# Performance work log

Measured on AMD Instinct MI355X. Metric: run time of the kernel, lower is better.

Reference implementation:

```python
import math
import jax, jax.numpy as jnp
import numpy as np

DIM = 512; DEPTH = 12; HEADS = 8; DIM_HEAD = 64
INNER = HEADS * DIM_HEAD
FF_INNER = 4 * DIM
B = 8192
NUM_TIMESTEPS = 1000
SCALE = 16.0  # cosine_sim_scale
ROT_DIM = 32  # RotaryEmbedding(dim=min(32, dim_head))
NUM_BUCKETS = 32; MAX_DISTANCE = 128


def layer_norm(x, g, eps=1e-5):
    mean = jnp.mean(x, axis=-1, keepdims=True)
    var = jnp.mean((x - mean) ** 2, axis=-1, keepdims=True)  # unbiased=False
    return (x - mean) * jax.lax.rsqrt(var + eps) * g


def l2norm(t):
    n = jnp.linalg.norm(t, axis=-1, keepdims=True)
    return t / jnp.maximum(n, 1e-12)


def rotary_freqs(n):
    inv = 1.0 / (10000.0 ** (jnp.arange(0, ROT_DIM, 2, dtype=jnp.float32) / ROT_DIM))
    f = jnp.arange(n, dtype=jnp.float32)[:, None] * inv[None, :]  # (n, ROT_DIM//2)
    return jnp.repeat(f, 2, axis=-1)  # (n, ROT_DIM), interleaved pairs


def rotate_half(x):
    x1 = x[..., 0::2]; x2 = x[..., 1::2]
    return jnp.stack((-x2, x1), axis=-1).reshape(x.shape)


def apply_rotary(t, freqs):
    tr, tp = t[..., :ROT_DIM], t[..., ROT_DIM:]
    tr = tr * jnp.cos(freqs) + rotate_half(tr) * jnp.sin(freqs)
    return jnp.concatenate([tr, tp], axis=-1)


def rel_pos_bias(i, j, emb):
    rel = jnp.arange(j)[None, :] - jnp.arange(i)[:, None]
    n = jnp.maximum(-rel, 0)
    max_exact = NUM_BUCKETS // 2
    nf = jnp.maximum(n, 1).astype(jnp.float32)
    val_large = max_exact + (jnp.log(nf / max_exact) / math.log(MAX_DISTANCE / max_exact) * (NUM_BUCKETS - max_exact)).astype(jnp.int32)
    val_large = jnp.minimum(val_large, NUM_BUCKETS - 1)
    bucket = jnp.where(n < max_exact, n, val_large)
    return emb[bucket].transpose(2, 0, 1)  # (h, i, j)


def setup_inputs() -> dict:
    key = jax.random.key(0)
    ks = jax.random.split(key, 13)
    w = 0.02
    return {
        "image_embed": jax.random.normal(ks[0], (B, DIM), jnp.float32),
        "text_embed": jax.random.normal(ks[1], (B, DIM), jnp.float32),
        "timesteps": jax.random.randint(ks[2], (B,), 0, NUM_TIMESTEPS),
        "time_emb_table": jax.random.normal(ks[3], (NUM_TIMESTEPS, DIM)) * w,
        "learned_query": jax.random.normal(ks[4], (DIM,)),
        "rel_emb": jax.random.normal(ks[5], (NUM_BUCKETS, HEADS)) * w,
        "attn_norm_g": jnp.ones((DEPTH, DIM)),
        "Wq": jax.random.normal(ks[6], (DEPTH, DIM, INNER)) * w,
        "Wkv": jax.random.normal(ks[7], (DEPTH, DIM, 2 * DIM_HEAD)) * w,
        "null_kv": jax.random.normal(ks[8], (DEPTH, 2, DIM_HEAD)),
        "Wo": jax.random.normal(ks[9], (DEPTH, INNER, DIM)) * w,
        "attn_out_norm_g": jnp.ones((DEPTH, DIM)),
        "ff_norm_g": jnp.ones((DEPTH, DIM)),
        "Wff1": jax.random.normal(ks[10], (DEPTH, DIM, 2 * FF_INNER)) * w,
        "Wff2": jax.random.normal(ks[11], (DEPTH, FF_INNER, DIM)) * w,
        "final_norm_g": jnp.ones((DIM,)),
        "Wproj": jax.random.normal(ks[12], (DIM, DIM)) * w,
    }


def reference(image_embed, text_embed, timesteps, time_emb_table, learned_query, rel_emb,
              attn_norm_g, Wq, Wkv, null_kv, Wo, attn_out_norm_g,
              ff_norm_g, Wff1, Wff2, final_norm_g, Wproj):
    b = image_embed.shape[0]
    # token sequence: [text_embed, time_embed, image_embed, learned_query] -> (b, 4, dim)
    tokens = jnp.concatenate([
        text_embed[:, None, :],
        time_emb_table[timesteps][:, None, :],
        image_embed[:, None, :],
        jnp.broadcast_to(learned_query, (b, 1, DIM)),
    ], axis=1)
    n = tokens.shape[1]
    bias = rel_pos_bias(n, n + 1, rel_emb)            # (h, n, n+1)
    freqs = rotary_freqs(n)                           # (n, ROT_DIM)
    causal = jnp.triu(jnp.ones((n, n + 1), dtype=bool), k=2)
    neg = -jnp.finfo(jnp.float32).max
    sqrt_scale = math.sqrt(SCALE)

    x = tokens
    for l in range(DEPTH):
        # --- Attention ---
        h = layer_norm(x, attn_norm_g[l])
        q = (h @ Wq[l]).reshape(b, n, HEADS, DIM_HEAD).transpose(0, 2, 1, 3) * SCALE
        kv = h @ Wkv[l]
        k, v = kv[..., :DIM_HEAD], kv[..., DIM_HEAD:]  # single-head kv (b, n, d)
        q = apply_rotary(q, freqs)
        k = apply_rotary(k, freqs)
        nk = jnp.broadcast_to(null_kv[l, 0], (b, 1, DIM_HEAD))
        nv = jnp.broadcast_to(null_kv[l, 1], (b, 1, DIM_HEAD))
        k = jnp.concatenate([nk, k], axis=1)
        v = jnp.concatenate([nv, v], axis=1)
        q = l2norm(q) * sqrt_scale
        k = l2norm(k) * sqrt_scale
        sim = jnp.einsum('bhid,bjd->bhij', q, k) + bias[None]
        sim = jnp.where(causal[None, None], neg, sim)
        attn = jax.nn.softmax(sim.astype(jnp.float32), axis=-1).astype(sim.dtype)
        out = jnp.einsum('bhij,bjd->bhid', attn, v).transpose(0, 2, 1, 3).reshape(b, n, INNER)
        x = x + layer_norm(out @ Wo[l], attn_out_norm_g[l])
        # --- SwiGLU FFN ---
        h = layer_norm(x, ff_norm_g[l])
        hg = h @ Wff1[l]
        a, g = hg[..., :FF_INNER], hg[..., FF_INNER:]
        x = x + (a * jax.nn.silu(g)) @ Wff2[l]

    x = layer_norm(x, final_norm_g) @ Wproj
    return x[:, -1, :]  # predicted image embed from learned query position
```

## Files before the change

kernel.cpp:

```cpp
#include <hip/hip_runtime.h>

typedef __bf16 bf16x8 __attribute__((ext_vector_type(8)));
typedef __bf16 bf16x2 __attribute__((ext_vector_type(2)));
typedef float  f32x4  __attribute__((ext_vector_type(4)));
typedef unsigned short u16;

#define BATCH   8192
#define NTOK    4
#define ROWS    (BATCH*NTOK)
#define DIM     512
#define HEADS   8
#define DH      64
#define FFI     2048
#define DEPTH   12
#define LN_EPS  1e-5f

static const size_t OFF_WQKV = 0;
static const size_t SZ_WQKV  = 12ull*640*512*2;
static const size_t OFF_WTO  = OFF_WQKV + SZ_WQKV;
static const size_t SZ_WTO   = 12ull*512*512*2;
static const size_t OFF_WTF1 = OFF_WTO + SZ_WTO;
static const size_t SZ_WTF1  = 12ull*4096*512*2;
static const size_t OFF_WTF2 = OFF_WTF1 + SZ_WTF1;
static const size_t SZ_WTF2  = 12ull*512*2048*2;
static const size_t OFF_WTP  = OFF_WTF2 + SZ_WTF2;
static const size_t SZ_WTP   = 512ull*512*2;
static const size_t OFF_X    = OFF_WTP + SZ_WTP;
static const size_t OFF_H    = OFF_X    + (size_t)ROWS*DIM*4;
static const size_t OFF_QKV  = OFF_H    + (size_t)ROWS*DIM*2;
static const size_t OFF_AO   = OFF_QKV  + (size_t)ROWS*640*2;
static const size_t OFF_FLAG = OFF_AO   + (size_t)ROWS*DIM*2;
static const size_t WS_NEED  = OFF_FLAG + 256;

__device__ __forceinline__ float ldf(const void* p, size_t i, bool b16) {
  return b16 ? (float)((const __bf16*)p)[i] : ((const float*)p)[i];
}

__device__ __forceinline__ void gld_lds16(const void* g, void* l) {
  __builtin_amdgcn_global_load_lds((const __attribute__((address_space(1))) void*)g,
                                   (__attribute__((address_space(3))) void*)l, 16, 0, 0);
}

__device__ __forceinline__ float wave_sum(float v) {
  #pragma unroll
  for (int o = 32; o > 0; o >>= 1) v += __shfl_xor(v, o, 64);
  return v;
}

__device__ __forceinline__ void block_reduce2(float& a, float& b, float* sm) {
  #pragma unroll
  for (int o = 32; o > 0; o >>= 1) { a += __shfl_down(a, o, 64); b += __shfl_down(b, o, 64); }
  int lane = threadIdx.x & 63, w = threadIdx.x >> 6;
  __syncthreads();
  if (lane == 0) { sm[w] = a; sm[4+w] = b; }
  __syncthreads();
  a = sm[0]+sm[1]+sm[2]+sm[3];
  b = sm[4]+sm[5]+sm[6]+sm[7];
}

__global__ void detect_dtype(const unsigned int* __restrict__ w, int* __restrict__ flag) {
  __shared__ int cnt[4];
  int t = threadIdx.x;
  int c = 0;
  for (int i = t; i < 2048; i += 256) {
    unsigned int v = w[i];
    unsigned int lo = v & 0xFFFFu, hi = v >> 16;
    int elo = (int)((lo >> 7) & 0xFF), ehi = (int)((hi >> 7) & 0xFF);
    bool okl = (lo == 0u) || (elo >= 100 && elo <= 140);
    bool okh = (hi == 0u) || (ehi >= 100 && ehi <= 140);
    if (okl && okh) c++;
  }
  #pragma unroll
  for (int o = 32; o > 0; o >>= 1) c += __shfl_down(c, o, 64);
  if ((t & 63) == 0) cnt[t >> 6] = c;
  __syncthreads();
  if (t == 0) flag[0] = (cnt[0] + cnt[1] + cnt[2] + cnt[3] > 1024) ? 1 : 0;
}

__global__ void transpose_any(const void* __restrict__ in, u16* __restrict__ out,
                              int K, int N, size_t out_zsz, int rowoff, int mode,
                              const int* __restrict__ flag) {
  bool b16 = flag[0] != 0;
  __shared__ u16 tile[32][33];
  size_t iboff = (size_t)blockIdx.z * K * N;
  size_t oboff = (size_t)blockIdx.z * out_zsz;
  int n0 = blockIdx.x * 32, k0 = blockIdx.y * 32;
  int tx = threadIdx.x, ty = threadIdx.y;
  #pragma unroll
  for (int r = 0; r < 4; r++) {
    float v = ldf(in, iboff + (size_t)(k0 + ty*4 + r) * N + n0 + tx, b16);
    __bf16 bv = (__bf16)v;
    tile[ty*4+r][tx] = __builtin_bit_cast(u16, bv);
  }
  __syncthreads();
  int rbase;
  if (mode == 0) rbase = rowoff + n0;
  else {
    int s = (n0 >= 2048) ? 1 : 0;
    int np = n0 - s*2048;
    rbase = (np >> 7)*256 + ((np >> 5) & 3)*64 + s*32;
  }
  #pragma unroll
  for (int r = 0; r < 4; r++)
    out[oboff + (size_t)(rbase + ty*4 + r) * K + k0 + tx] = tile[tx][ty*4+r];
}

__global__ void build_tokens(const void* __restrict__ text, const void* __restrict__ img,
                             const int* __restrict__ ts, const void* __restrict__ table,
                             const void* __restrict__ lq, float* __restrict__ x,
                             const int* __restrict__ flag) {
  bool b16 = flag[0] != 0;
  int b = blockIdx.x, t = threadIdx.x;
  float* xr = x + (size_t)b * NTOK * DIM;
  int tsb = ts[b];
  for (int e = t; e < DIM; e += 256) {
    xr[e]         = ldf(text,  (size_t)b * DIM + e, b16);
    xr[DIM + e]   = ldf(table, (size_t)tsb * DIM + e, b16);
    xr[2*DIM + e] = ldf(img,   (size_t)b * DIM + e, b16);
    xr[3*DIM + e] = ldf(lq,    (size_t)e, b16);
  }
}

__global__ void ln_f32_bf16(const float* __restrict__ x, const void* __restrict__ g, size_t goff,
                            __bf16* __restrict__ out, const int* __restrict__ flag) {
  bool b16 = flag[0] != 0;
  __shared__ float sm[8];
  int row = blockIdx.x, t = threadIdx.x;
  float2 v = ((const float2*)(x + (size_t)row * DIM))[t];
  float s = v.x + v.y, s2 = v.x*v.x + v.y*v.y;
  block_reduce2(s, s2, sm);
  float mean = s * (1.f/DIM);
  float var  = s2 * (1.f/DIM) - mean*mean;
  float rs = rsqrtf(var + LN_EPS);
  float g0 = ldf(g, goff + 2*t, b16), g1 = ldf(g, goff + 2*t + 1, b16);
  bf16x2 o2 = { (__bf16)((v.x-mean)*rs*g0), (__bf16)((v.y-mean)*rs*g1) };
  ((bf16x2*)(out + (size_t)row * DIM))[t] = o2;
}

__global__ void ln_add_ln(const __bf16* __restrict__ y,
                          const void* __restrict__ g1, size_t g1off,
                          const void* __restrict__ g2, size_t g2off,
                          float* __restrict__ x, __bf16* __restrict__ h,
                          const int* __restrict__ flag) {
  bool b16 = flag[0] != 0;
  __shared__ float sm[8];
  int row = blockIdx.x, t = threadIdx.x;
  bf16x2 yv = ((const bf16x2*)(y + (size_t)row * DIM))[t];
  float v0 = (float)yv[0], v1 = (float)yv[1];
  float s = v0 + v1, s2 = v0*v0 + v1*v1;
  block_reduce2(s, s2, sm);
  float mean = s * (1.f/DIM);
  float var  = s2 * (1.f/DIM) - mean*mean;
  float rs = rsqrtf(var + LN_EPS);
  float ga = ldf(g1, g1off + 2*t, b16), gb = ldf(g1, g1off + 2*t + 1, b16);
  float2* xr = (float2*)(x + (size_t)row * DIM);
  float2 xv = xr[t];
  xv.x += (v0-mean)*rs*ga;
  xv.y += (v1-mean)*rs*gb;
  xr[t] = xv;
  float s_  = xv.x + xv.y, s2_ = xv.x*xv.x + xv.y*xv.y;
  block_reduce2(s_, s2_, sm);
  float mean2 = s_ * (1.f/DIM);
  float var2  = s2_ * (1.f/DIM) - mean2*mean2;
  float rs2 = rsqrtf(var2 + LN_EPS);
  float gc = ldf(g2, g2off + 2*t, b16), gd = ldf(g2, g2off + 2*t + 1, b16);
  bf16x2 o2 = { (__bf16)((xv.x-mean2)*rs2*gc), (__bf16)((xv.y-mean2)*rs2*gd) };
  ((bf16x2*)(h + (size_t)row * DIM))[t] = o2;
}

__global__ void ln_final(const float* __restrict__ x, const void* __restrict__ g,
                         __bf16* __restrict__ out, const int* __restrict__ flag) {
  bool b16 = flag[0] != 0;
  __shared__ float sm[8];
  int b = blockIdx.x, t = threadIdx.x;
  int row = b*NTOK + 3;
  float2 v = ((const float2*)(x + (size_t)row * DIM))[t];
  float s = v.x + v.y, s2 = v.x*v.x + v.y*v.y;
  block_reduce2(s, s2, sm);
  float mean = s * (1.f/DIM);
  float var  = s2 * (1.f/DIM) - mean*mean;
  float rs = rsqrtf(var + LN_EPS);
  float g0 = ldf(g, (size_t)2*t, b16), g1 = ldf(g, (size_t)2*t + 1, b16);
  bf16x2 o2 = { (__bf16)((v.x-mean)*rs*g0), (__bf16)((v.y-mean)*rs*g1) };
  ((bf16x2*)(out + (size_t)b * DIM))[t] = o2;
}

template<int MODE>
__global__ __launch_bounds__(256) void gemm_bt(
    const __bf16* __restrict__ A, int lda,
    const __bf16* __restrict__ B, int ldb,
    void* __restrict__ Cv, int ldc, int K, const int* __restrict__ flag)
{
  __shared__ __bf16 As[128*64];
  __shared__ __bf16 Bs[128*64];
  const int tid = threadIdx.x;
  const int bx = blockIdx.x, by = blockIdx.y;
  const int wave = tid >> 6, lane = tid & 63;
  const int wr = wave >> 1, wc = wave & 1;
  const __bf16* Ab = A + (size_t)by * 128 * lda;
  const __bf16* Bb = B + (size_t)bx * 128 * ldb;
  f32x4 acc[4][4] = {};
  const int srow = tid >> 3;
  const int scs  = ((tid & 7) ^ (srow & 7)) * 8;
  const int lr = lane & 15, lc = lane >> 4;
  for (int k0 = 0; k0 < K; k0 += 64) {
    __syncthreads();
    #pragma unroll
    for (int s = 0; s < 4; s++) {
      gld_lds16(Ab + (size_t)(s*32 + srow)*lda + k0 + scs, (char*)As + s*4096 + wave*1024);
      gld_lds16(Bb + (size_t)(s*32 + srow)*ldb + k0 + scs, (char*)Bs + s*4096 + wave*1024);
    }
    __syncthreads();
    #pragma unroll
    for (int kk = 0; kk < 2; kk++) {
      bf16x8 af[4], bq[4];
      #pragma unroll
      for (int m = 0; m < 4; m++)
        af[m] = *(const bf16x8*)(As + (wr*64 + m*16 + lr)*64 + (((kk*4 + lc) ^ (lr & 7)) * 8));
      #pragma unroll
      for (int n = 0; n < 4; n++)
        bq[n] = *(const bf16x8*)(Bs + (wc*64 + n*16 + lr)*64 + (((kk*4 + lc) ^ (lr & 7)) * 8));
      #pragma unroll
      for (int m = 0; m < 4; m++)
        #pragma unroll
        for (int n = 0; n < 4; n++)
          acc[m][n] = __builtin_amdgcn_mfma_f32_16x16x32_bf16(af[m], bq[n], acc[m][n], 0, 0, 0);
    }
  }
  const int row0 = by*128 + wr*64 + (lane >> 4)*4;
  const int col0 = bx*128 + wc*64 + (lane & 15);
  if (MODE == 0) {
    __bf16* Cb = (__bf16*)Cv;
    #pragma unroll
    for (int m = 0; m < 4; m++)
      #pragma unroll
      for (int rr = 0; rr < 4; rr++) {
        size_t ro = (size_t)(row0 + m*16 + rr) * ldc + col0;
        #pragma unroll
        for (int n = 0; n < 4; n++) Cb[ro + n*16] = (__bf16)acc[m][n][rr];
      }
  } else {
    bool b16o = flag[0] != 0;
    __bf16* Cb = (__bf16*)Cv;
    float*  Cf = (float*)Cv;
    #pragma unroll
    for (int m = 0; m < 4; m++)
      #pragma unroll
      for (int rr = 0; rr < 4; rr++) {
        size_t ro = (size_t)(row0 + m*16 + rr) * ldc + col0;
        #pragma unroll
        for (int n = 0; n < 4; n++) {
          float val = acc[m][n][rr];
          if (b16o) Cb[ro + n*16] = (__bf16)val; else Cf[ro + n*16] = val;
        }
      }
  }
}

template<int BROWS, int EPI>
__global__ __launch_bounds__(512, 2) void gemm8(
    const __bf16* __restrict__ A, int lda,
    const __bf16* __restrict__ B, int ldb,
    void* __restrict__ Cv, int ldc, int K)
{
  constexpr int UNITS = (BROWS == 256) ? 4 : 3;
  constexpr int WCN   = (BROWS == 256) ? 4 : 2;
  constexpr int M_FR  = (BROWS == 256) ? 8 : 4;
  constexpr int QM    = M_FR / 4;
  __shared__ char ldsmem[2][(256 + BROWS) * 128];

  const int tid = threadIdx.x;
  const int wid = tid >> 6, lane = tid & 63;
  const int wr = wid / WCN, wc = wid % WCN;
  const int lr = lane & 15, lc = lane >> 4;
  const int sr = tid >> 3;
  const int cs = ((tid & 7) ^ (sr & 7)) * 8;
  const int bx = blockIdx.x, by = blockIdx.y;

  const __bf16* Ab = A + (size_t)by * 256 * lda;
  const __bf16* Bb = B + (size_t)bx * BROWS * ldb;

  f32x4 acc[M_FR][4] = {};
  const int NT = K >> 6;

  char* lds0 = ldsmem[0];
  char* lds1 = ldsmem[1];

  auto stage_unit = [&](int p, int kt, int u) {
    char* base = (p ? lds1 : lds0);
    if (u < 2) {
      const __bf16* s = Ab + (size_t)(u*128 + sr) * lda + kt*64 + cs;
      char* d = base + u*16384 + (wid << 10);
      gld_lds16(s, d);
      gld_lds16(s + (size_t)64 * lda, d + 8192);
    } else {
      const __bf16* s = Bb + (size_t)((u-2)*128 + sr) * ldb + kt*64 + cs;
      char* d = base + 32768 + (u-2)*16384 + (wid << 10);
      gld_lds16(s, d);
      gld_lds16(s + (size_t)64 * ldb, d + 8192);
    }
  };

  #pragma unroll
  for (int u = 0; u < UNITS; u++) stage_unit(0, 0, u);

  const int NIT = NT >> 1;
  for (int i = 0; i < NIT; i++) {
    const int t1 = 2*i + 1;
    const int t2 = (2*i + 2 < NT) ? (2*i + 2) : 0;
    #pragma unroll
    for (int hfl = 0; hfl < 2; hfl++) {
      char* cbase = hfl ? lds1 : lds0;
      const int sp = hfl ^ 1;
      const int st = hfl ? t2 : t1;
      bf16x8 bfr[4][2];
      #pragma unroll
      for (int q = 0; q < 4; q++) {
        if (q < UNITS) stage_unit(sp, st, q);
        if (q == 0) {
          asm volatile("s_waitcnt vmcnt(2)" ::: "memory");
          asm volatile("s_barrier" ::: "memory");
          #pragma unroll
          for (int f = 0; f < 4; f++)
            #pragma unroll
            for (int kk = 0; kk < 2; kk++) {
              int row = wc*64 + f*16 + lr;
              int ch = (kk*4 + lc) ^ (lr & 7);
              bfr[f][kk] = *(const bf16x8*)(cbase + 32768 + row*128 + ch*16);
            }
        }
        bf16x8 afr[QM][2];
        #pragma unroll
        for (int m2 = 0; m2 < QM; m2++)
          #pragma unroll
          for (int kk = 0; kk < 2; kk++) {
            int row = wr*(M_FR*16) + (q*QM + m2)*16 + lr;
            int ch = (kk*4 + lc) ^ (lr & 7);
            afr[m2][kk] = *(const bf16x8*)(cbase + row*128 + ch*16);
          }
        __builtin_amdgcn_s_setprio(1);
        #pragma unroll
        for (int m2 = 0; m2 < QM; m2++)
          #pragma unroll
          for (int n = 0; n < 4; n++)
            #pragma unroll
            for (int kk = 0; kk < 2; kk++)
              acc[q*QM + m2][n] = __builtin_amdgcn_mfma_f32_16x16x32_bf16(
                  afr[m2][kk], bfr[n][kk], acc[q*QM + m2][n], 0, 0, 0);
        __builtin_amdgcn_s_setprio(0);
        asm volatile("s_barrier" ::: "memory");
      }
    }
  }

  if (EPI == 1) {
    __bf16* Ob = (__bf16*)Cv;
    const int colb = bx*128 + wc*32 + lr;
    const int rowb = by*256 + wr*128 + lc*4;
    #pragma unroll
    for (int m = 0; m < M_FR; m++)
      #pragma unroll
      for (int rr = 0; rr < 4; rr++) {
        size_t ro = (size_t)(rowb + m*16 + rr) * ldc;
        #pragma unroll
        for (int fa = 0; fa < 2; fa++) {
          float a = acc[m][fa][rr], g = acc[m][fa+2][rr];
          Ob[ro + colb + fa*16] = (__bf16)(a * g / (1.f + __expf(-g)));
        }
      }
  } else {
    float* Xf = (float*)Cv;
    const int colb = bx*BROWS + wc*64 + lr;
    const int rowb = by*256 + wr*(M_FR*16) + lc*4;
    #pragma unroll
    for (int m = 0; m < M_FR; m++)
      #pragma unroll
      for (int rr = 0; rr < 4; rr++) {
        size_t ro = (size_t)(rowb + m*16 + rr) * ldc;
        #pragma unroll
        for (int n = 0; n < 4; n++) Xf[ro + colb + n*16] += acc[m][n][rr];
      }
  }
}

__global__ __launch_bounds__(256) void attn_kernel(
    const __bf16* __restrict__ qkv,
    const void* __restrict__ nkv_all, int layer, const void* __restrict__ rel_emb,
    __bf16* __restrict__ ao, const int* __restrict__ flag)
{
  bool b16 = flag[0] != 0;
  int gw = blockIdx.x * 4 + (threadIdx.x >> 6);
  int lane = threadIdx.x & 63;
  int b = gw >> 3, h = gw & 7;
  int d = lane;
  bool rot = d < 32;
  int j2 = d >> 1;
  float inv = __expf(-(float)(2*j2) * (1.f/32.f) * 9.210340371976184f);

  float sn[4], cn[4];
  #pragma unroll
  for (int t2 = 0; t2 < 4; t2++) __sincosf((float)t2 * inv, &sn[t2], &cn[t2]);
  float rb[4];
  #pragma unroll
  for (int t2 = 0; t2 < 4; t2++) rb[t2] = ldf(rel_emb, (size_t)t2 * 8 + h, b16);

  float q[4];
  #pragma unroll
  for (int i = 0; i < 4; i++) {
    float v = (float)qkv[((size_t)(b*NTOK + i)) * 640 + h*DH + d];
    float p = __shfl_xor(v, 1, 64);
    if (rot) v = (d & 1) ? (v*cn[i] + p*sn[i]) : (v*cn[i] - p*sn[i]);
    q[i] = v;
  }
  #pragma unroll
  for (int i = 0; i < 4; i++) {
    float nrm = sqrtf(wave_sum(q[i]*q[i]));
    q[i] = q[i] / fmaxf(nrm, 1e-12f);
  }

  float kk[5], vv[5];
  kk[0] = ldf(nkv_all, (size_t)layer*128 + d, b16);
  vv[0] = ldf(nkv_all, (size_t)layer*128 + 64 + d, b16);
  #pragma unroll
  for (int j = 1; j < 5; j++) {
    const __bf16* base = qkv + ((size_t)(b*NTOK + j - 1)) * 640 + 512;
    float v = (float)base[d];
    vv[j] = (float)base[64 + d];
    float p = __shfl_xor(v, 1, 64);
    if (rot) v = (d & 1) ? (v*cn[j-1] + p*sn[j-1]) : (v*cn[j-1] - p*sn[j-1]);
    kk[j] = v;
  }
  #pragma unroll
  for (int j = 0; j < 5; j++) {
    float nrm = sqrtf(wave_sum(kk[j]*kk[j]));
    kk[j] = kk[j] / fmaxf(nrm, 1e-12f);
  }

  #pragma unroll
  for (int i = 0; i < 4; i++) {
    float sim[5];
    #pragma unroll
    for (int j = 0; j < 5; j++) {
      if (j > i + 1) break;
      float p = wave_sum(q[i] * kk[j]);
      sim[j] = p * 16.f + rb[(i - j > 0) ? (i - j) : 0];
    }
    float m = sim[0];
    #pragma unroll
    for (int j = 1; j < 5; j++) { if (j > i + 1) break; m = fmaxf(m, sim[j]); }
    float Z = 0.f, o = 0.f;
    #pragma unroll
    for (int j = 0; j < 5; j++) {
      if (j > i + 1) break;
      float e = __expf(sim[j] - m);
      Z += e; o += e * vv[j];
    }
    ao[((size_t)(b*NTOK + i)) * DIM + h*DH + d] = (__bf16)(o / Z);
  }
}

extern "C" void kernel_launch(void* const* d_in, const int* in_sizes, int n_in,
                              void* d_out, int out_size, void* d_ws, size_t ws_size,
                              hipStream_t stream) {
  const void* image_embed     = d_in[0];
  const void* text_embed      = d_in[1];
  const int*  timesteps       = (const int*)d_in[2];
  const void* time_table      = d_in[3];
  const void* learned_query   = d_in[4];
  const void* rel_emb         = d_in[5];
  const void* attn_norm_g     = d_in[6];
  const void* Wq              = d_in[7];
  const void* Wkv             = d_in[8];
  const void* null_kv         = d_in[9];
  const void* Wo              = d_in[10];
  const void* attn_out_norm_g = d_in[11];
  const void* ff_norm_g       = d_in[12];
  const void* Wff1            = d_in[13];
  const void* Wff2            = d_in[14];
  const void* final_norm_g    = d_in[15];
  const void* Wproj           = d_in[16];

  if (ws_size < WS_NEED) return;

  char* ws = (char*)d_ws;
  __bf16* wqkv = (__bf16*)(ws + OFF_WQKV);
  __bf16* wto  = (__bf16*)(ws + OFF_WTO);
  __bf16* wtf1 = (__bf16*)(ws + OFF_WTF1);
  __bf16* wtf2 = (__bf16*)(ws + OFF_WTF2);
  __bf16* wtp  = (__bf16*)(ws + OFF_WTP);
  float*  x    = (float*) (ws + OFF_X);
  __bf16* h    = (__bf16*)(ws + OFF_H);
  __bf16* qkv  = (__bf16*)(ws + OFF_QKV);
  __bf16* ao   = (__bf16*)(ws + OFF_AO);
  __bf16* act  = (__bf16*)(ws + OFF_QKV);
  int*    flag = (int*)   (ws + OFF_FLAG);

  detect_dtype<<<1, 256, 0, stream>>>((const unsigned int*)Wq, flag);

  dim3 tb(32, 8);
  transpose_any<<<dim3(16, 16, 12),  tb, 0, stream>>>(Wq,   (u16*)wqkv, 512,  512,  640ull*512, 0,   0, flag);
  transpose_any<<<dim3(4,  16, 12),  tb, 0, stream>>>(Wkv,  (u16*)wqkv, 512,  128,  640ull*512, 512, 0, flag);
  transpose_any<<<dim3(16, 16, 12),  tb, 0, stream>>>(Wo,   (u16*)wto,  512,  512,  512ull*512, 0,   0, flag);
  transpose_any<<<dim3(128,16, 12),  tb, 0, stream>>>(Wff1, (u16*)wtf1, 512,  4096, 4096ull*512,0,   1, flag);
  transpose_any<<<dim3(16, 64, 12),  tb, 0, stream>>>(Wff2, (u16*)wtf2, 2048, 512,  512ull*2048,0,   0, flag);
  transpose_any<<<dim3(16, 16, 1),   tb, 0, stream>>>(Wproj,(u16*)wtp,  512,  512,  512ull*512, 0,   0, flag);

  build_tokens<<<BATCH, 256, 0, stream>>>(text_embed, image_embed, timesteps, time_table,
                                          learned_query, x, flag);

  for (int l = 0; l < DEPTH; l++) {
    const __bf16* wqkv_l = wqkv + (size_t)l * 640 * 512;
    const __bf16* wto_l  = wto  + (size_t)l * 512 * 512;
    const __bf16* wtf1_l = wtf1 + (size_t)l * 4096 * 512;
    const __bf16* wtf2_l = wtf2 + (size_t)l * 512 * 2048;

    ln_f32_bf16<<<ROWS, 256, 0, stream>>>(x, attn_norm_g, (size_t)l*DIM, h, flag);
    gemm_bt<0><<<dim3(5, ROWS/128), 256, 0, stream>>>(h, DIM, wqkv_l, 512, qkv, 640, 512, flag);
    attn_kernel<<<BATCH*HEADS/4, 256, 0, stream>>>(qkv, null_kv, l, rel_emb, ao, flag);
    gemm_bt<0><<<dim3(4, ROWS/128), 256, 0, stream>>>(ao, DIM, wto_l, 512, qkv , DIM, 512, flag);
    ln_add_ln<<<ROWS, 256, 0, stream>>>(qkv , attn_out_norm_g, (size_t)l*DIM,
                                        ff_norm_g, (size_t)l*DIM, x, h, flag);

    for (int c = 0; c < 2; c++) {
      const __bf16* hc = h + (size_t)c * 16384 * DIM;
      float*        xc = x + (size_t)c * 16384 * DIM;
      gemm8<256,1><<<dim3(16, 64), 512, 0, stream>>>(hc, DIM, wtf1_l, 512, act, FFI, 512);
      gemm8<128,2><<<dim3(4, 64), 512, 0, stream>>>(act, FFI, wtf2_l, FFI, xc, DIM, 2048);
    }
  }

  ln_final<<<BATCH, 256, 0, stream>>>(x, final_norm_g, ao , flag);
  gemm_bt<2><<<dim3(4, BATCH/128), 256, 0, stream>>>(ao, DIM, wtp, 512, d_out, DIM, 512, flag);
}
```

Baseline: 6.172 ms.

## Replace small gemm_bt with gemm8 tiles and vectorize attention to 16 lanes per head

Removes the 128x128 gemm_bt kernel and routes the QKV, output-projection and final projection GEMMs through the larger 256x128 gemm8 kernel, adding bf16 and flag-dependent output epilogues. The attention kernel now handles each (batch, head) with a 16-lane group, each lane holding 4 elements, so reductions take 4 shuffle steps instead of 6 and loads and stores are 8-byte vectors. The aim is better GEMM efficiency from larger tiles with pipelined loads, and less shuffle and launch overhead in attention. Larger tiles mean fewer blocks for these small-N GEMMs, which may hurt occupancy.

```diff
diff --git a/kernel.cpp b/kernel.cpp
--- a/kernel.cpp
+++ b/kernel.cpp
@@ -1,6 +1,7 @@
 #include <hip/hip_runtime.h>
 
 typedef __bf16 bf16x8 __attribute__((ext_vector_type(8)));
+typedef __bf16 bf16x4 __attribute__((ext_vector_type(4)));
 typedef __bf16 bf16x2 __attribute__((ext_vector_type(2)));
 typedef float  f32x4  __attribute__((ext_vector_type(4)));
 typedef unsigned short u16;
@@ -41,9 +42,9 @@
                                    (__attribute__((address_space(3))) void*)l, 16, 0, 0);
 }
 
-__device__ __forceinline__ float wave_sum(float v) {
-  #pragma unroll
-  for (int o = 32; o > 0; o >>= 1) v += __shfl_xor(v, o, 64);
+__device__ __forceinline__ float gsum16(float v) {
+  #pragma unroll
+  for (int o = 8; o > 0; o >>= 1) v += __shfl_xor(v, o, 64);
   return v;
 }
 
@@ -185,83 +186,11 @@
   ((bf16x2*)(out + (size_t)b * DIM))[t] = o2;
 }
 
-template<int MODE>
-__global__ __launch_bounds__(256) void gemm_bt(
-    const __bf16* __restrict__ A, int lda,
-    const __bf16* __restrict__ B, int ldb,
-    void* __restrict__ Cv, int ldc, int K, const int* __restrict__ flag)
-{
-  __shared__ __bf16 As[128*64];
-  __shared__ __bf16 Bs[128*64];
-  const int tid = threadIdx.x;
-  const int bx = blockIdx.x, by = blockIdx.y;
-  const int wave = tid >> 6, lane = tid & 63;
-  const int wr = wave >> 1, wc = wave & 1;
-  const __bf16* Ab = A + (size_t)by * 128 * lda;
-  const __bf16* Bb = B + (size_t)bx * 128 * ldb;
-  f32x4 acc[4][4] = {};
-  const int srow = tid >> 3;
-  const int scs  = ((tid & 7) ^ (srow & 7)) * 8;
-  const int lr = lane & 15, lc = lane >> 4;
-  for (int k0 = 0; k0 < K; k0 += 64) {
-    __syncthreads();
-    #pragma unroll
-    for (int s = 0; s < 4; s++) {
-      gld_lds16(Ab + (size_t)(s*32 + srow)*lda + k0 + scs, (char*)As + s*4096 + wave*1024);
-      gld_lds16(Bb + (size_t)(s*32 + srow)*ldb + k0 + scs, (char*)Bs + s*4096 + wave*1024);
-    }
-    __syncthreads();
-    #pragma unroll
-    for (int kk = 0; kk < 2; kk++) {
-      bf16x8 af[4], bq[4];
-      #pragma unroll
-      for (int m = 0; m < 4; m++)
-        af[m] = *(const bf16x8*)(As + (wr*64 + m*16 + lr)*64 + (((kk*4 + lc) ^ (lr & 7)) * 8));
-      #pragma unroll
-      for (int n = 0; n < 4; n++)
-        bq[n] = *(const bf16x8*)(Bs + (wc*64 + n*16 + lr)*64 + (((kk*4 + lc) ^ (lr & 7)) * 8));
-      #pragma unroll
-      for (int m = 0; m < 4; m++)
-        #pragma unroll
-        for (int n = 0; n < 4; n++)
-          acc[m][n] = __builtin_amdgcn_mfma_f32_16x16x32_bf16(af[m], bq[n], acc[m][n], 0, 0, 0);
-    }
-  }
-  const int row0 = by*128 + wr*64 + (lane >> 4)*4;
-  const int col0 = bx*128 + wc*64 + (lane & 15);
-  if (MODE == 0) {
-    __bf16* Cb = (__bf16*)Cv;
-    #pragma unroll
-    for (int m = 0; m < 4; m++)
-      #pragma unroll
-      for (int rr = 0; rr < 4; rr++) {
-        size_t ro = (size_t)(row0 + m*16 + rr) * ldc + col0;
-        #pragma unroll
-        for (int n = 0; n < 4; n++) Cb[ro + n*16] = (__bf16)acc[m][n][rr];
-      }
-  } else {
-    bool b16o = flag[0] != 0;
-    __bf16* Cb = (__bf16*)Cv;
-    float*  Cf = (float*)Cv;
-    #pragma unroll
-    for (int m = 0; m < 4; m++)
-      #pragma unroll
-      for (int rr = 0; rr < 4; rr++) {
-        size_t ro = (size_t)(row0 + m*16 + rr) * ldc + col0;
-        #pragma unroll
-        for (int n = 0; n < 4; n++) {
-          float val = acc[m][n][rr];
-          if (b16o) Cb[ro + n*16] = (__bf16)val; else Cf[ro + n*16] = val;
-        }
-      }
-  }
-}
-
 template<int BROWS, int EPI>
 __global__ __launch_bounds__(512, 2) void gemm8(
     const __bf16* __restrict__ A, int lda,
     const __bf16* __restrict__ B, int ldb,
-    void* __restrict__ Cv, int ldc, int K)
+    void* __restrict__ Cv, int ldc, int K, const int* __restrict__ flag)
 {
   constexpr int UNITS = (BROWS == 256) ? 4 : 3;
   constexpr int WCN   = (BROWS == 256) ? 4 : 2;
@@ -368,7 +297,7 @@
           Ob[ro + colb + fa*16] = (__bf16)(a * g / (1.f + __expf(-g)));
         }
       }
-  } else {
+  } else if (EPI == 2) {
     float* Xf = (float*)Cv;
     const int colb = bx*BROWS + wc*64 + lr;
     const int rowb = by*256 + wr*(M_FR*16) + lc*4;
@@ -380,6 +309,35 @@
         #pragma unroll
         for (int n = 0; n < 4; n++) Xf[ro + colb + n*16] += acc[m][n][rr];
       }
+  } else if (EPI == 0) {
+    __bf16* Cb = (__bf16*)Cv;
+    const int colb = bx*BROWS + wc*64 + lr;
+    const int rowb = by*256 + wr*(M_FR*16) + lc*4;
+    #pragma unroll
+    for (int m = 0; m < M_FR; m++)
+      #pragma unroll
+      for (int rr = 0; rr < 4; rr++) {
+        size_t ro = (size_t)(rowb + m*16 + rr) * ldc;
+        #pragma unroll
+        for (int n = 0; n < 4; n++) Cb[ro + colb + n*16] = (__bf16)acc[m][n][rr];
+      }
+  } else {
+    bool b16o = flag[0] != 0;
+    __bf16* Cb = (__bf16*)Cv;
+    float*  Cf = (float*)Cv;
+    const int colb = bx*BROWS + wc*64 + lr;
+    const int rowb = by*256 + wr*(M_FR*16) + lc*4;
+    #pragma unroll
+    for (int m = 0; m < M_FR; m++)
+      #pragma unroll
+      for (int rr = 0; rr < 4; rr++) {
+        size_t ro = (size_t)(rowb + m*16 + rr) * ldc;
+        #pragma unroll
+        for (int n = 0; n < 4; n++) {
+          float val = acc[m][n][rr];
+          if (b16o) Cb[ro + colb + n*16] = (__bf16)val; else Cf[ro + colb + n*16] = val;
+        }
+      }
   }
 }
 
@@ -389,51 +347,74 @@
     __bf16* __restrict__ ao, const int* __restrict__ flag)
 {
   bool b16 = flag[0] != 0;
-  int gw = blockIdx.x * 4 + (threadIdx.x >> 6);
-  int lane = threadIdx.x & 63;
-  int b = gw >> 3, h = gw & 7;
-  int d = lane;
-  bool rot = d < 32;
-  int j2 = d >> 1;
-  float inv = __expf(-(float)(2*j2) * (1.f/32.f) * 9.210340371976184f);
-
-  float sn[4], cn[4];
-  #pragma unroll
-  for (int t2 = 0; t2 < 4; t2++) __sincosf((float)t2 * inv, &sn[t2], &cn[t2]);
+  const int tid = threadIdx.x;
+  const int w = tid >> 6, l = tid & 63;
+  const int g = l >> 4, c = l & 15;
+  const int bh = blockIdx.x * 16 + w * 4 + g;
+  const int b = bh >> 3, h = bh & 7;
+  const bool rot = (c < 8);
+
+  const float LN1E4_32 = 9.210340371976184f * (1.f/32.f);
+  float inv0 = __expf(-(float)(4*c)     * LN1E4_32);
+  float inv1 = __expf(-(float)(4*c + 2) * LN1E4_32);
+  float cs0[4], sn0[4], cs1[4], sn1[4];
+  #pragma unroll
+  for (int t = 0; t < 4; t++) {
+    __sincosf((float)t * inv0, &sn0[t], &cs0[t]);
+    __sincosf((float)t * inv1, &sn1[t], &cs1[t]);
+  }
   float rb[4];
   #pragma unroll
-  for (int t2 = 0; t2 < 4; t2++) rb[t2] = ldf(rel_emb, (size_t)t2 * 8 + h, b16);
-
-  float q[4];
+  for (int t = 0; t < 4; t++) rb[t] = ldf(rel_emb, (size_t)t * 8 + h, b16);
+
+  float q[4][4];
   #pragma unroll
   for (int i = 0; i < 4; i++) {
-    float v = (float)qkv[((size_t)(b*NTOK + i)) * 640 + h*DH + d];
-    float p = __shfl_xor(v, 1, 64);
-    if (rot) v = (d & 1) ? (v*cn[i] + p*sn[i]) : (v*cn[i] - p*sn[i]);
-    q[i] = v;
+    bf16x4 qv = *(const bf16x4*)(qkv + ((size_t)(b*NTOK + i)) * 640 + h*DH + c*4);
+    float v0 = (float)qv[0], v1 = (float)qv[1], v2 = (float)qv[2], v3 = (float)qv[3];
+    if (rot) {
+      float n0 = v0*cs0[i] - v1*sn0[i], n1 = v1*cs0[i] + v0*sn0[i];
+      float n2 = v2*cs1[i] - v3*sn1[i], n3 = v3*cs1[i] + v2*sn1[i];
+      v0 = n0; v1 = n1; v2 = n2; v3 = n3;
+    }
+    q[i][0] = v0; q[i][1] = v1; q[i][2] = v2; q[i][3] = v3;
   }
   #pragma unroll
   for (int i = 0; i < 4; i++) {
-    float nrm = sqrtf(wave_sum(q[i]*q[i]));
-    q[i] = q[i] / fmaxf(nrm, 1e-12f);
-  }
-
-  float kk[5], vv[5];
-  kk[0] = ldf(nkv_all, (size_t)layer*128 + d, b16);
-  vv[0] = ldf(nkv_all, (size_t)layer*128 + 64 + d, b16);
+    float ss = q[i][0]*q[i][0] + q[i][1]*q[i][1] + q[i][2]*q[i][2] + q[i][3]*q[i][3];
+    float r = 1.f / fmaxf(sqrtf(gsum16(ss)), 1e-12f);
+    #pragma unroll
+    for (int e = 0; e < 4; e++) q[i][e] *= r;
+  }
+
+  float kk[5][4], vv[5][4];
+  #pragma unroll
+  for (int e = 0; e < 4; e++) {
+    kk[0][e] = ldf(nkv_all, (size_t)layer*128 + c*4 + e, b16);
+    vv[0][e] = ldf(nkv_all, (size_t)layer*128 + 64 + c*4 + e, b16);
+  }
   #pragma unroll
   for (int j = 1; j < 5; j++) {
     const __bf16* base = qkv + ((size_t)(b*NTOK + j - 1)) * 640 + 512;
-    float v = (float)base[d];
-    vv[j] = (float)base[64 + d];
-    float p = __shfl_xor(v, 1, 64);
-    if (rot) v = (d & 1) ? (v*cn[j-1] + p*sn[j-1]) : (v*cn[j-1] - p*sn[j-1]);
-    kk[j] = v;
+    bf16x4 kv4 = *(const bf16x4*)(base + c*4);
+    bf16x4 vv4 = *(const bf16x4*)(base + 64 + c*4);
+    float v0 = (float)kv4[0], v1 = (float)kv4[1], v2 = (float)kv4[2], v3 = (float)kv4[3];
+    if (rot) {
+      int t = j - 1;
+      float n0 = v0*cs0[t] - v1*sn0[t], n1 = v1*cs0[t] + v0*sn0[t];
+      float n2 = v2*cs1[t] - v3*sn1[t], n3 = v3*cs1[t] + v2*sn1[t];
+      v0 = n0; v1 = n1; v2 = n2; v3 = n3;
+    }
+    kk[j][0] = v0; kk[j][1] = v1; kk[j][2] = v2; kk[j][3] = v3;
+    #pragma unroll
+    for (int e = 0; e < 4; e++) vv[j][e] = (float)vv4[e];
   }
   #pragma unroll
   for (int j = 0; j < 5; j++) {
-    float nrm = sqrtf(wave_sum(kk[j]*kk[j]));
-    kk[j] = kk[j] / fmaxf(nrm, 1e-12f);
+    float ss = kk[j][0]*kk[j][0] + kk[j][1]*kk[j][1] + kk[j][2]*kk[j][2] + kk[j][3]*kk[j][3];
+    float r = 1.f / fmaxf(sqrtf(gsum16(ss)), 1e-12f);
+    #pragma unroll
+    for (int e = 0; e < 4; e++) kk[j][e] *= r;
   }
 
   #pragma unroll
@@ -442,20 +423,23 @@
     #pragma unroll
     for (int j = 0; j < 5; j++) {
       if (j > i + 1) break;
-      float p = wave_sum(q[i] * kk[j]);
-      sim[j] = p * 16.f + rb[(i - j > 0) ? (i - j) : 0];
+      float pp = q[i][0]*kk[j][0] + q[i][1]*kk[j][1] + q[i][2]*kk[j][2] + q[i][3]*kk[j][3];
+      sim[j] = 16.f * gsum16(pp) + rb[(i - j > 0) ? (i - j) : 0];
     }
     float m = sim[0];
     #pragma unroll
     for (int j = 1; j < 5; j++) { if (j > i + 1) break; m = fmaxf(m, sim[j]); }
-    float Z = 0.f, o = 0.f;
+    float Z = 0.f, o0 = 0.f, o1 = 0.f, o2 = 0.f, o3 = 0.f;
     #pragma unroll
     for (int j = 0; j < 5; j++) {
       if (j > i + 1) break;
       float e = __expf(sim[j] - m);
-      Z += e; o += e * vv[j];
-    }
-    ao[((size_t)(b*NTOK + i)) * DIM + h*DH + d] = (__bf16)(o / Z);
+      Z += e;
+      o0 += e * vv[j][0]; o1 += e * vv[j][1]; o2 += e * vv[j][2]; o3 += e * vv[j][3];
+    }
+    float rz = 1.f / Z;
+    bf16x4 ov = { (__bf16)(o0*rz), (__bf16)(o1*rz), (__bf16)(o2*rz), (__bf16)(o3*rz) };
+    *(bf16x4*)(ao + ((size_t)(b*NTOK + i)) * DIM + h*DH + c*4) = ov;
   }
 }
 
@@ -515,20 +499,20 @@
     const __bf16* wtf2_l = wtf2 + (size_t)l * 512 * 2048;
 
     ln_f32_bf16<<<ROWS, 256, 0, stream>>>(x, attn_norm_g, (size_t)l*DIM, h, flag);
-    gemm_bt<0><<<dim3(5, ROWS/128), 256, 0, stream>>>(h, DIM, wqkv_l, 512, qkv, 640, 512, flag);
-    attn_kernel<<<BATCH*HEADS/4, 256, 0, stream>>>(qkv, null_kv, l, rel_emb, ao, flag);
-    gemm_bt<0><<<dim3(4, ROWS/128), 256, 0, stream>>>(ao, DIM, wto_l, 512, qkv , DIM, 512, flag);
+    gemm8<128,0><<<dim3(5, 128), 512, 0, stream>>>(h, DIM, wqkv_l, 512, qkv, 640, 512, flag);
+    attn_kernel<<<BATCH/2, 256, 0, stream>>>(qkv, null_kv, l, rel_emb, ao, flag);
+    gemm8<128,0><<<dim3(4, 128), 512, 0, stream>>>(ao, DIM, wto_l, 512, qkv , DIM, 512, flag);
     ln_add_ln<<<ROWS, 256, 0, stream>>>(qkv , attn_out_norm_g, (size_t)l*DIM,
                                         ff_norm_g, (size_t)l*DIM, x, h, flag);
 
     for (int c = 0; c < 2; c++) {
       const __bf16* hc = h + (size_t)c * 16384 * DIM;
       float*        xc = x + (size_t)c * 16384 * DIM;
-      gemm8<256,1><<<dim3(16, 64), 512, 0, stream>>>(hc, DIM, wtf1_l, 512, act, FFI, 512);
-      gemm8<128,2><<<dim3(4, 64), 512, 0, stream>>>(act, FFI, wtf2_l, FFI, xc, DIM, 2048);
+      gemm8<256,1><<<dim3(16, 64), 512, 0, stream>>>(hc, DIM, wtf1_l, 512, act, FFI, 512, flag);
+      gemm8<128,2><<<dim3(4, 64), 512, 0, stream>>>(act, FFI, wtf2_l, FFI, xc, DIM, 2048, flag);
     }
   }
 
   ln_final<<<BATCH, 256, 0, stream>>>(x, final_norm_g, ao , flag);
-  gemm_bt<2><<<dim3(4, BATCH/128), 256, 0, stream>>>(ao, DIM, wtp, 512, d_out, DIM, 512, flag);
-}
+  gemm8<128,3><<<dim3(4, 32), 512, 0, stream>>>(ao, DIM, wtp, 512, d_out, DIM, 512, flag);
+}
```

Result: faster. 5.390 ms (median of 2 runs) (-12.7%).
